# Kernel tuning notes

Hardware: AMD Instinct MI355X
Metric: run time of the kernel (lower is better)

The kernel has to match this reference:

```python
import math
import jax, jax.numpy as jnp
import numpy as np

NEG_INF_FILL = 1e-09  # faithful to the source: masked positions get +1e-09, not -inf

B, H, S, D = 2, 16, 2048, 64


def setup_inputs() -> dict:
    key = jax.random.key(0)
    kq, kk, kv = jax.random.split(key, 3)
    q = jax.random.normal(kq, (B, H, S, D), dtype=jnp.float32)
    k = jax.random.normal(kk, (B, H, S, D), dtype=jnp.float32)
    v = jax.random.normal(kv, (B, H, S, D), dtype=jnp.float32)
    # causal boolean mask, broadcast over heads: [B, 1, S, S]
    causal = jnp.tril(jnp.ones((S, S), dtype=bool))
    attention_mask = jnp.broadcast_to(causal[None, None, :, :], (B, 1, S, S))
    return {"q": q, "k": k, "v": v, "attention_mask": attention_mask}


def reference(q, k, v, attention_mask):
    d_k = q.shape[-1]
    # scores: [B, H, S, S]
    scores = jnp.einsum("bhqd,bhkd->bhqk", q, k) / math.sqrt(d_k)
    scores = jnp.where(attention_mask, scores, NEG_INF_FILL)
    attn = jax.nn.softmax(scores, axis=-1)
    # output: [B, H, S, D]
    return jnp.einsum("bhqk,bhkd->bhqd", attn, v)
```

## Files before the change

### kernel.cpp

```cpp
#include <hip/hip_runtime.h>


#define SEQ 2048
#define DIM 64
#define NKT 32
#define QSCALE 0.18033688011112042f

typedef _Float16 half_t;
typedef _Float16 half8  __attribute__((ext_vector_type(8)));
typedef _Float16 half4v __attribute__((ext_vector_type(4)));
typedef _Float16 half2v __attribute__((ext_vector_type(2)));
typedef float    float4v __attribute__((ext_vector_type(4)));

#define KIMG_HALFS ((size_t)4194304)
#define WS_NEED    ((size_t)17039360)

__device__ __forceinline__ void glds16(const void* g, void* l) {
    __builtin_amdgcn_global_load_lds((const __attribute__((address_space(1))) void*)g,
                                     (__attribute__((address_space(3))) void*)l,
                                     16, 0, 0);
}

__global__ __launch_bounds__(256)
void prep_kernel(const float* __restrict__ K, const float* __restrict__ V,
                 half_t* __restrict__ Kimg, half_t* __restrict__ Vimg) {
    __shared__ __align__(16) half_t vt[64 * 72];
    const int kt = blockIdx.x, bh = blockIdx.y;
    const int tid = threadIdx.x;
    const float* Kt = K + ((size_t)bh * SEQ + kt * 64) * DIM;
    const float* Vt = V + ((size_t)bh * SEQ + kt * 64) * DIM;
    half_t* Kd = Kimg + (((size_t)(bh * NKT + kt)) << 12);
    half_t* Vd = Vimg + (((size_t)(bh * NKT + kt)) << 12);

    {
        const int row = tid >> 2, q = tid & 3;
        const float* src = Kt + row * DIM + 16 * q;
        #pragma unroll
        for (int cc = 0; cc < 2; ++cc) {
            float4v a = *(const float4v*)(src + 8 * cc);
            float4v b = *(const float4v*)(src + 8 * cc + 4);
            half8 hh;
            hh[0]=(half_t)a[0]; hh[1]=(half_t)a[1]; hh[2]=(half_t)a[2]; hh[3]=(half_t)a[3];
            hh[4]=(half_t)b[0]; hh[5]=(half_t)b[1]; hh[6]=(half_t)b[2]; hh[7]=(half_t)b[3];
            const int sc = (2 * q + cc) ^ (row & 7);
            *(half8*)(Kd + row * 64 + sc * 8) = hh;
        }
    }
    {
        const int c = tid & 15, r0 = tid >> 4;
        #pragma unroll
        for (int u = 0; u < 2; ++u) {
            const float* vp = Vt + (size_t)(2 * (r0 + 16 * u)) * DIM + 4 * c;
            float4v x0 = *(const float4v*)(vp);
            float4v x1 = *(const float4v*)(vp + DIM);
            #pragma unroll
            for (int i = 0; i < 4; ++i) {
                const int d = 4 * c + i;
                vt[d * 72 + 2 * (r0 + 16 * u)]     = (half_t)x0[i];
                vt[d * 72 + 2 * (r0 + 16 * u) + 1] = (half_t)x1[i];
            }
        }
    }
    __syncthreads();
    {
        const int d = tid >> 2, g = tid & 3;
        #pragma unroll
        for (int cc = 0; cc < 2; ++cc) {
            const int c0 = 2 * g + cc;
            half8 hh = *(const half8*)(vt + d * 72 + 8 * c0);
            const int sc = c0 ^ (d & 7);
            *(half8*)(Vd + d * 64 + sc * 8) = hh;
        }
    }
}

__global__ __launch_bounds__(256)
void suffix_kernel(const float* __restrict__ V, float* __restrict__ Stab) {
    __shared__ float part[32 * 9];
    const int dg = blockIdx.x, bh = blockIdx.y;
    const int t = threadIdx.x >> 3, dl = threadIdx.x & 7;
    const int d = dg * 8 + dl;
    const float* Vb = V + (size_t)bh * SEQ * DIM;
    float s = 0.f;
    #pragma unroll 8
    for (int j = 0; j < 64; ++j) s += Vb[(size_t)(t * 64 + j) * DIM + d];
    part[t * 9 + dl] = s;
    __syncthreads();
    float r = 0.f;
    for (int tt = 31; tt >= t; --tt) r += part[tt * 9 + dl];
    Stab[((size_t)bh * 32 + t) * 64 + d] = r;
}

__global__ __launch_bounds__(256, 4)
void attn_mfma_kernel(const float* __restrict__ Q,
                      const half_t* __restrict__ Kimg,
                      const half_t* __restrict__ Vimg,
                      const float* __restrict__ Stab,
                      float* __restrict__ O) {
    __shared__ __align__(16) half_t smem_h[20480];

    const int tid = threadIdx.x;
    const int l   = tid & 63;
    const int w   = tid >> 6;
    const int lx  = l & 15;
    const int h   = l >> 4;
    const int bh  = blockIdx.x;
    const int qb  = 31 - (int)blockIdx.y;
    const int qbase = qb * 64;
    const int nkt = qb + 1;
    const int n_tail = SEQ - nkt * 64;

    const float* Qh = Q + (size_t)bh * SEQ * DIM;
    float*       Oh = O + (size_t)bh * SEQ * DIM;

    half8 qf[2];
    const int qrow_w = qbase + 16 * w;
    {
        const float* qp = Qh + (size_t)(qrow_w + lx) * DIM;
        #pragma unroll
        for (int s = 0; s < 2; ++s) {
            float4v a = *(const float4v*)(qp + 32 * s + 8 * h);
            float4v b = *(const float4v*)(qp + 32 * s + 8 * h + 4);
            half8 f;
            f[0] = (half_t)(a[0] * QSCALE); f[1] = (half_t)(a[1] * QSCALE);
            f[2] = (half_t)(a[2] * QSCALE); f[3] = (half_t)(a[3] * QSCALE);
            f[4] = (half_t)(b[0] * QSCALE); f[5] = (half_t)(b[1] * QSCALE);
            f[6] = (half_t)(b[2] * QSCALE); f[7] = (half_t)(b[3] * QSCALE);
            qf[s] = f;
        }
    }

    float4v acc[4];
    #pragma unroll
    for (int mt = 0; mt < 4; ++mt) acc[mt] = (float4v){0.f, 0.f, 0.f, 0.f};
    float lp = 0.f;

    const size_t tile0 = ((size_t)(bh * NKT)) << 13;
    auto stage = [&](int kt, int buf) {
        const size_t toff = tile0 + ((size_t)kt << 13);
        const char* gk = (const char*)Kimg + toff + (tid << 4);
        const char* gv = (const char*)Vimg + toff + (tid << 4);
        char* lk = (char*)smem_h + (buf << 13) + (w << 10);
        char* lv = (char*)smem_h + 16384 + (buf << 13) + (w << 10);
        glds16(gk, lk);  glds16(gk + 4096, lk + 4096);
        glds16(gv, lv);  glds16(gv + 4096, lv + 4096);
    };

    const int sx  = lx & 7;
    const int o0h = (h ^ sx) << 3;
    const int o1h = ((h + 4) ^ sx) << 3;
    half_t* Psw = smem_h + 16384 + (w << 10);

    stage(0, 0);
    asm volatile("s_waitcnt vmcnt(0)" ::: "memory");
    __syncthreads();

    int cur = 0;
    for (int kt = 0; kt < nkt; ++kt) {
        if (kt + 1 < nkt) stage(kt + 1, cur ^ 1);

        const half_t* Kb = smem_h + cur * 4096 + (lx << 6);
        const half_t* Vb = smem_h + 8192 + cur * 4096 + (lx << 6);
        const int key_base = kt << 6;

        #pragma unroll
        for (int mt = 0; mt < 4; ++mt) {
            half8 ak0 = *(const half8*)(Kb + (mt << 10) + o0h);
            half8 ak1 = *(const half8*)(Kb + (mt << 10) + o1h);
            float4v ct = (float4v){0.f, 0.f, 0.f, 0.f};
            ct = __builtin_amdgcn_mfma_f32_16x16x32_f16(ak0, qf[0], ct, 0, 0, 0);
            ct = __builtin_amdgcn_mfma_f32_16x16x32_f16(ak1, qf[1], ct, 0, 0, 0);
            float p[4];
            #pragma unroll
            for (int r = 0; r < 4; ++r)
                p[r] = __builtin_amdgcn_exp2f(ct[r]);
            if ((key_base + 16 * mt + 15) > qrow_w) {
                const int qg = qrow_w + lx;
                const int kb = key_base + 16 * mt + 4 * h;
                #pragma unroll
                for (int r = 0; r < 4; ++r)
                    if (kb + r > qg) p[r] = 1.0f;
            }
            lp += (p[0] + p[1]) + (p[2] + p[3]);
            half4v hp;
            hp[0] = (half_t)p[0]; hp[1] = (half_t)p[1];
            hp[2] = (half_t)p[2]; hp[3] = (half_t)p[3];
            *(half4v*)(Psw + (lx << 6)
                       + ((((mt << 1) + (h >> 1)) ^ sx) << 3) + ((h & 1) << 2)) = hp;
        }

        half8 pf0 = *(const half8*)(Psw + (lx << 6) + o0h);
        half8 pf1 = *(const half8*)(Psw + (lx << 6) + o1h);
        #pragma unroll
        for (int mtd = 0; mtd < 4; ++mtd) {
            half8 av0 = *(const half8*)(Vb + (mtd << 10) + o0h);
            half8 av1 = *(const half8*)(Vb + (mtd << 10) + o1h);
            float4v ct = acc[mtd];
            ct = __builtin_amdgcn_mfma_f32_16x16x32_f16(av0, pf0, ct, 0, 0, 0);
            ct = __builtin_amdgcn_mfma_f32_16x16x32_f16(av1, pf1, ct, 0, 0, 0);
            acc[mtd] = ct;
        }

        asm volatile("s_waitcnt vmcnt(0)" ::: "memory");
        __syncthreads();
        cur ^= 1;
    }

    float s_l = lp;
    s_l += __shfl_xor(s_l, 16, 64);
    s_l += __shfl_xor(s_l, 32, 64);
    const float linv = 1.0f / (s_l + (float)n_tail);

    float vt_l[4][4];
    if (n_tail > 0) {
        const float* Sr = Stab + (((size_t)bh << 5) + nkt) * 64;
        #pragma unroll
        for (int mt = 0; mt < 4; ++mt) {
            float4v x = *(const float4v*)(Sr + 16 * mt + 4 * h);
            vt_l[mt][0] = x[0]; vt_l[mt][1] = x[1];
            vt_l[mt][2] = x[2]; vt_l[mt][3] = x[3];
        }
    } else {
        #pragma unroll
        for (int mt = 0; mt < 4; ++mt)
            vt_l[mt][0] = vt_l[mt][1] = vt_l[mt][2] = vt_l[mt][3] = 0.f;
    }

    float* Osm = (float*)smem_h;
    #pragma unroll
    for (int mt = 0; mt < 4; ++mt)
        #pragma unroll
        for (int r = 0; r < 4; ++r) {
            float o = (acc[mt][r] + vt_l[mt][r]) * linv;
            Osm[w * (16 * 65) + lx * 65 + 16 * mt + 4 * h + r] = o;
        }
    __syncthreads();
    {
        const int c = tid & 15, r0 = tid >> 4;
        #pragma unroll
        for (int u = 0; u < 4; ++u) {
            const int row = r0 + 16 * u;
            const int dc = 4 * c;
            const float* src = Osm + (row >> 4) * (16 * 65) + (row & 15) * 65 + dc;
            float4v ov = {src[0], src[1], src[2], src[3]};
            *(float4v*)(Oh + (size_t)(qbase + row) * DIM + dc) = ov;
        }
    }
}

#define KS_STRIDE 72
#define PS_STRIDE 72

__global__ __launch_bounds__(256, 4)
void attn_mfma_fallback(const float* __restrict__ Q,
                        const float* __restrict__ K,
                        const float* __restrict__ V,
                        float* __restrict__ O) {
    __shared__ half_t smem_h[64 * KS_STRIDE + 64 * KS_STRIDE + 4 * 16 * PS_STRIDE];
    half_t* Ks  = smem_h;
    half_t* VTs = smem_h + 64 * KS_STRIDE;
    half_t* Ps  = smem_h + 2 * 64 * KS_STRIDE;

    const int tid = threadIdx.x;
    const int l   = tid & 63;
    const int w   = tid >> 6;
    const int lx  = l & 15;
    const int h   = l >> 4;
    const int bh  = blockIdx.x;
    const int qb  = 31 - (int)blockIdx.y;
    const int qbase = qb * 64;
    const int nkt = qb + 1;
    const int n_tail = SEQ - nkt * 64;

    const float* Qh = Q + (size_t)bh * SEQ * DIM;
    const float* Kh = K + (size_t)bh * SEQ * DIM;
    const float* Vh = V + (size_t)bh * SEQ * DIM;
    float*       Oh = O + (size_t)bh * SEQ * DIM;

    half8 qf[2];
    const int qrow_w = qbase + 16 * w;
    {
        const float* qp = Qh + (size_t)(qrow_w + lx) * DIM;
        #pragma unroll
        for (int s = 0; s < 2; ++s) {
            float4v a = *(const float4v*)(qp + 32 * s + 8 * h);
            float4v b = *(const float4v*)(qp + 32 * s + 8 * h + 4);
            half8 f;
            f[0] = (half_t)(a[0] * QSCALE); f[1] = (half_t)(a[1] * QSCALE);
            f[2] = (half_t)(a[2] * QSCALE); f[3] = (half_t)(a[3] * QSCALE);
            f[4] = (half_t)(b[0] * QSCALE); f[5] = (half_t)(b[1] * QSCALE);
            f[6] = (half_t)(b[2] * QSCALE); f[7] = (half_t)(b[3] * QSCALE);
            qf[s] = f;
        }
    }

    float4v acc[4];
    #pragma unroll
    for (int mt = 0; mt < 4; ++mt) acc[mt] = (float4v){0.f, 0.f, 0.f, 0.f};
    float lp = 0.f;

    const int c  = tid & 15;
    const int r0 = tid >> 4;

    float4v kreg[4], vreg[4];
    auto load_tile = [&](int kt) {
        const float* Kt = Kh + (size_t)kt * 64 * DIM;
        const float* Vt = Vh + (size_t)kt * 64 * DIM;
        #pragma unroll
        for (int u = 0; u < 4; ++u)
            kreg[u] = *(const float4v*)(Kt + (r0 + 16 * u) * DIM + 4 * c);
        #pragma unroll
        for (int u = 0; u < 2; ++u) {
            const float* vp = Vt + (size_t)(2 * (r0 + 16 * u)) * DIM + 4 * c;
            vreg[2 * u]     = *(const float4v*)(vp);
            vreg[2 * u + 1] = *(const float4v*)(vp + DIM);
        }
    };

    load_tile(0);

    for (int kt = 0; kt < nkt; ++kt) {
        __syncthreads();
        #pragma unroll
        for (int u = 0; u < 4; ++u) {
            int kr = r0 + 16 * u;
            half4v hk;
            hk[0] = (half_t)kreg[u][0]; hk[1] = (half_t)kreg[u][1];
            hk[2] = (half_t)kreg[u][2]; hk[3] = (half_t)kreg[u][3];
            *(half4v*)(Ks + kr * KS_STRIDE + 4 * c) = hk;
        }
        #pragma unroll
        for (int u = 0; u < 2; ++u) {
            int kp = r0 + 16 * u;
            #pragma unroll
            for (int i = 0; i < 4; ++i) {
                int ir = (i + c + (c >> 2)) & 3;
                int dr = 4 * c + ir;
                half2v hv;
                hv[0] = (half_t)vreg[2 * u][ir];
                hv[1] = (half_t)vreg[2 * u + 1][ir];
                *(half2v*)(VTs + dr * KS_STRIDE + 2 * kp) = hv;
            }
        }
        __syncthreads();

        if (kt + 1 < nkt) load_tile(kt + 1);

        const int key_base = kt * 64;
        #pragma unroll
        for (int mt = 0; mt < 4; ++mt) {
            half8 ak0 = *(const half8*)(Ks + (16 * mt + lx) * KS_STRIDE + 8 * h);
            half8 ak1 = *(const half8*)(Ks + (16 * mt + lx) * KS_STRIDE + 32 + 8 * h);
            const bool need_mask = (key_base + 16 * mt + 15) > qrow_w;
            float4v ct = (float4v){0.f, 0.f, 0.f, 0.f};
            ct = __builtin_amdgcn_mfma_f32_16x16x32_f16(ak0, qf[0], ct, 0, 0, 0);
            ct = __builtin_amdgcn_mfma_f32_16x16x32_f16(ak1, qf[1], ct, 0, 0, 0);
            float p[4];
            #pragma unroll
            for (int r = 0; r < 4; ++r)
                p[r] = __builtin_amdgcn_exp2f(ct[r]);
            if (need_mask) {
                const int qg = qrow_w + lx;
                const int kb = key_base + 16 * mt + 4 * h;
                #pragma unroll
                for (int r = 0; r < 4; ++r)
                    if (kb + r > qg) p[r] = 1.0f;
            }
            lp += (p[0] + p[1]) + (p[2] + p[3]);
            half4v hp;
            hp[0] = (half_t)p[0]; hp[1] = (half_t)p[1];
            hp[2] = (half_t)p[2]; hp[3] = (half_t)p[3];
            *(half4v*)(Ps + w * (16 * PS_STRIDE) + lx * PS_STRIDE + 16 * mt + 4 * h) = hp;
        }

        half8 pf[2];
        #pragma unroll
        for (int s = 0; s < 2; ++s)
            pf[s] = *(const half8*)(Ps + w * (16 * PS_STRIDE) + lx * PS_STRIDE
                                    + 32 * s + 8 * h);
        #pragma unroll
        for (int mtd = 0; mtd < 4; ++mtd) {
            half8 av0 = *(const half8*)(VTs + (16 * mtd + lx) * KS_STRIDE + 8 * h);
            half8 av1 = *(const half8*)(VTs + (16 * mtd + lx) * KS_STRIDE + 32 + 8 * h);
            float4v ct = acc[mtd];
            ct = __builtin_amdgcn_mfma_f32_16x16x32_f16(av0, pf[0], ct, 0, 0, 0);
            ct = __builtin_amdgcn_mfma_f32_16x16x32_f16(av1, pf[1], ct, 0, 0, 0);
            acc[mtd] = ct;
        }
    }

    float s_l = lp;
    s_l += __shfl_xor(s_l, 16, 64);
    s_l += __shfl_xor(s_l, 32, 64);
    const float linv = 1.0f / (s_l + (float)n_tail);

    float ts0 = 0.f, ts1 = 0.f, ts2 = 0.f, ts3 = 0.f;
    {
        const int tstart = nkt * 64;
        #pragma unroll 4
        for (int k = tstart + r0; k < SEQ; k += 16) {
            float4v x = *(const float4v*)(Vh + (size_t)k * DIM + 4 * c);
            ts0 += x[0]; ts1 += x[1]; ts2 += x[2]; ts3 += x[3];
        }
    }
    __syncthreads();
    float* preS = (float*)smem_h;
    float* vtf  = ((float*)smem_h) + 4160;
    {
        float4v pv = {ts0, ts1, ts2, ts3};
        *(float4v*)(preS + r0 * 68 + 4 * c) = pv;
    }
    __syncthreads();
    if (tid < 64) {
        float s = 0.f;
        #pragma unroll
        for (int p = 0; p < 16; ++p) s += preS[p * 68 + tid];
        vtf[tid] = s;
    }
    __syncthreads();
    float vt_l[4][4];
    #pragma unroll
    for (int mt = 0; mt < 4; ++mt)
        #pragma unroll
        for (int r = 0; r < 4; ++r) vt_l[mt][r] = vtf[16 * mt + 4 * h + r];

    float* Osm = (float*)smem_h;
    #pragma unroll
    for (int mt = 0; mt < 4; ++mt)
        #pragma unroll
        for (int r = 0; r < 4; ++r) {
            float o = (acc[mt][r] + vt_l[mt][r]) * linv;
            Osm[w * (16 * 65) + lx * 65 + 16 * mt + 4 * h + r] = o;
        }
    __syncthreads();
    #pragma unroll
    for (int u = 0; u < 4; ++u) {
        int row = r0 + 16 * u;
        int dc = 4 * c;
        const float* src = Osm + (row >> 4) * (16 * 65) + (row & 15) * 65 + dc;
        float4v ov = {src[0], src[1], src[2], src[3]};
        *(float4v*)(Oh + (size_t)(qbase + row) * DIM + dc) = ov;
    }
}

extern "C" void kernel_launch(void* const* d_in, const int* in_sizes, int n_in,
                              void* d_out, int out_size, void* d_ws, size_t ws_size,
                              hipStream_t stream) {
    const float* q = (const float*)d_in[0];
    const float* k = (const float*)d_in[1];
    const float* v = (const float*)d_in[2];
    float* out = (float*)d_out;

    if (d_ws != nullptr && ws_size >= WS_NEED) {
        half_t* kimg = (half_t*)d_ws;
        half_t* vimg = kimg + KIMG_HALFS;
        float*  stab = (float*)((char*)d_ws + 16777216);
        prep_kernel<<<dim3(32, 32), 256, 0, stream>>>(k, v, kimg, vimg);
        suffix_kernel<<<dim3(8, 32), 256, 0, stream>>>(v, stab);
        attn_mfma_kernel<<<dim3(32, 32), 256, 0, stream>>>(q, kimg, vimg, stab, out);
    } else {
        attn_mfma_fallback<<<dim3(32, 32), 256, 0, stream>>>(q, k, v, out);
    }
}
```

Baseline: 150.0 us.

## Pair causal query blocks per workgroup and fuse suffix-sum into prep kernel

The attention kernel now runs 512 workgroups, each handling two query blocks (qb = 31-p and qb = p), so every workgroup does the same number of causal key tiles. This replaces a grid of 1024 blocks with very uneven work. The separate suffix-sum kernel is folded into the prep kernel as extra blocks, which removes one launch. In exchange, each workgroup now processes its two query blocks one after the other, and the grid is half as large, which may lower occupancy and latency hiding.

```diff
diff --git a/kernel.cpp b/kernel.cpp
--- a/kernel.cpp
+++ b/kernel.cpp
@@ -23,10 +23,30 @@
 
 __global__ __launch_bounds__(256)
 void prep_kernel(const float* __restrict__ K, const float* __restrict__ V,
-                 half_t* __restrict__ Kimg, half_t* __restrict__ Vimg) {
+                 half_t* __restrict__ Kimg, half_t* __restrict__ Vimg,
+                 float* __restrict__ Stab) {
     __shared__ __align__(16) half_t vt[64 * 72];
-    const int kt = blockIdx.x, bh = blockIdx.y;
+    __shared__ float part[32 * 9];
+    const int bh = blockIdx.y;
     const int tid = threadIdx.x;
+
+    if (blockIdx.x >= NKT) {
+        const int dg = blockIdx.x - NKT;
+        const int t = tid >> 3, dl = tid & 7;
+        const int d = dg * 8 + dl;
+        const float* Vb = V + (size_t)bh * SEQ * DIM;
+        float s = 0.f;
+        #pragma unroll 8
+        for (int j = 0; j < 64; ++j) s += Vb[(size_t)(t * 64 + j) * DIM + d];
+        part[t * 9 + dl] = s;
+        __syncthreads();
+        float r = 0.f;
+        for (int tt = 31; tt >= t; --tt) r += part[tt * 9 + dl];
+        Stab[((size_t)bh * 32 + t) * 64 + d] = r;
+        return;
+    }
+
+    const int kt = blockIdx.x;
     const float* Kt = K + ((size_t)bh * SEQ + kt * 64) * DIM;
     const float* Vt = V + ((size_t)bh * SEQ + kt * 64) * DIM;
     half_t* Kd = Kimg + (((size_t)(bh * NKT + kt)) << 12);
@@ -74,23 +94,6 @@
     }
 }
 
-__global__ __launch_bounds__(256)
-void suffix_kernel(const float* __restrict__ V, float* __restrict__ Stab) {
-    __shared__ float part[32 * 9];
-    const int dg = blockIdx.x, bh = blockIdx.y;
-    const int t = threadIdx.x >> 3, dl = threadIdx.x & 7;
-    const int d = dg * 8 + dl;
-    const float* Vb = V + (size_t)bh * SEQ * DIM;
-    float s = 0.f;
-    #pragma unroll 8
-    for (int j = 0; j < 64; ++j) s += Vb[(size_t)(t * 64 + j) * DIM + d];
-    part[t * 9 + dl] = s;
-    __syncthreads();
-    float r = 0.f;
-    for (int tt = 31; tt >= t; --tt) r += part[tt * 9 + dl];
-    Stab[((size_t)bh * 32 + t) * 64 + d] = r;
-}
-
 __global__ __launch_bounds__(256, 4)
 void attn_mfma_kernel(const float* __restrict__ Q,
                       const half_t* __restrict__ Kimg,
@@ -98,6 +101,173 @@
                       const float* __restrict__ Stab,
                       float* __restrict__ O) {
     __shared__ __align__(16) half_t smem_h[20480];
+
+    const int tid = threadIdx.x;
+    const int l   = tid & 63;
+    const int w   = tid >> 6;
+    const int lx  = l & 15;
+    const int h   = l >> 4;
+    const int bh  = blockIdx.x;
+    const int p   = blockIdx.y;
+
+    const float* Qh = Q + (size_t)bh * SEQ * DIM;
+    float*       Oh = O + (size_t)bh * SEQ * DIM;
+
+    const size_t tile0 = ((size_t)(bh * NKT)) << 13;
+    auto stage = [&](int kt, int buf) {
+        const size_t toff = tile0 + ((size_t)kt << 13);
+        const char* gk = (const char*)Kimg + toff + (tid << 4);
+        const char* gv = (const char*)Vimg + toff + (tid << 4);
+        char* lk = (char*)smem_h + (buf << 13) + (w << 10);
+        char* lv = (char*)smem_h + 16384 + (buf << 13) + (w << 10);
+        glds16(gk, lk);  glds16(gk + 4096, lk + 4096);
+        glds16(gv, lv);  glds16(gv + 4096, lv + 4096);
+    };
+
+    const int sx  = lx & 7;
+    const int o0h = (h ^ sx) << 3;
+    const int o1h = ((h + 4) ^ sx) << 3;
+    half_t* Psw = smem_h + 16384 + (w << 10);
+
+    for (int seg = 0; seg < 2; ++seg) {
+        const int qb    = seg ? p : 31 - p;
+        const int qbase = qb << 6;
+        const int nkt   = qb + 1;
+        const int n_tail = SEQ - (nkt << 6);
+        const int qrow_w = qbase + 16 * w;
+
+        half8 qf[2];
+        {
+            const float* qp = Qh + (size_t)(qrow_w + lx) * DIM;
+            #pragma unroll
+            for (int s = 0; s < 2; ++s) {
+                float4v a = *(const float4v*)(qp + 32 * s + 8 * h);
+                float4v b = *(const float4v*)(qp + 32 * s + 8 * h + 4);
+                half8 f;
+                f[0] = (half_t)(a[0] * QSCALE); f[1] = (half_t)(a[1] * QSCALE);
+                f[2] = (half_t)(a[2] * QSCALE); f[3] = (half_t)(a[3] * QSCALE);
+                f[4] = (half_t)(b[0] * QSCALE); f[5] = (half_t)(b[1] * QSCALE);
+                f[6] = (half_t)(b[2] * QSCALE); f[7] = (half_t)(b[3] * QSCALE);
+                qf[s] = f;
+            }
+        }
+
+        float4v acc[4];
+        #pragma unroll
+        for (int mt = 0; mt < 4; ++mt) acc[mt] = (float4v){0.f, 0.f, 0.f, 0.f};
+        float lp = 0.f;
+
+        __syncthreads();
+        stage(0, 0);
+        asm volatile("s_waitcnt vmcnt(0)" ::: "memory");
+        __syncthreads();
+
+        int cur = 0;
+        for (int kt = 0; kt < nkt; ++kt) {
+            if (kt + 1 < nkt) stage(kt + 1, cur ^ 1);
+
+            const half_t* Kb = smem_h + cur * 4096 + (lx << 6);
+            const half_t* Vb = smem_h + 8192 + cur * 4096 + (lx << 6);
+            const int key_base = kt << 6;
+
+            #pragma unroll
+            for (int mt = 0; mt < 4; ++mt) {
+                half8 ak0 = *(const half8*)(Kb + (mt << 10) + o0h);
+                half8 ak1 = *(const half8*)(Kb + (mt << 10) + o1h);
+                float4v ct = (float4v){0.f, 0.f, 0.f, 0.f};
+                ct = __builtin_amdgcn_mfma_f32_16x16x32_f16(ak0, qf[0], ct, 0, 0, 0);
+                ct = __builtin_amdgcn_mfma_f32_16x16x32_f16(ak1, qf[1], ct, 0, 0, 0);
+                float pv[4];
+                #pragma unroll
+                for (int r = 0; r < 4; ++r)
+                    pv[r] = __builtin_amdgcn_exp2f(ct[r]);
+                if ((key_base + 16 * mt + 15) > qrow_w) {
+                    const int qg = qrow_w + lx;
+                    const int kb = key_base + 16 * mt + 4 * h;
+                    #pragma unroll
+                    for (int r = 0; r < 4; ++r)
+                        if (kb + r > qg) pv[r] = 1.0f;
+                }
+                lp += (pv[0] + pv[1]) + (pv[2] + pv[3]);
+                half4v hp;
+                hp[0] = (half_t)pv[0]; hp[1] = (half_t)pv[1];
+                hp[2] = (half_t)pv[2]; hp[3] = (half_t)pv[3];
+                *(half4v*)(Psw + (lx << 6)
+                           + ((((mt << 1) + (h >> 1)) ^ sx) << 3) + ((h & 1) << 2)) = hp;
+            }
+
+            half8 pf0 = *(const half8*)(Psw + (lx << 6) + o0h);
+            half8 pf1 = *(const half8*)(Psw + (lx << 6) + o1h);
+            #pragma unroll
+            for (int mtd = 0; mtd < 4; ++mtd) {
+                half8 av0 = *(const half8*)(Vb + (mtd << 10) + o0h);
+                half8 av1 = *(const half8*)(Vb + (mtd << 10) + o1h);
+                float4v ct = acc[mtd];
+                ct = __builtin_amdgcn_mfma_f32_16x16x32_f16(av0, pf0, ct, 0, 0, 0);
+                ct = __builtin_amdgcn_mfma_f32_16x16x32_f16(av1, pf1, ct, 0, 0, 0);
+                acc[mtd] = ct;
+            }
+
+            asm volatile("s_waitcnt vmcnt(0)" ::: "memory");
+            __syncthreads();
+            cur ^= 1;
+        }
+
+        float s_l = lp;
+        s_l += __shfl_xor(s_l, 16, 64);
+        s_l += __shfl_xor(s_l, 32, 64);
+        const float linv = 1.0f / (s_l + (float)n_tail);
+
+        float vt_l[4][4];
+        if (n_tail > 0) {
+            const float* Sr = Stab + (((size_t)bh << 5) + nkt) * 64;
+            #pragma unroll
+            for (int mt = 0; mt < 4; ++mt) {
+                float4v x = *(const float4v*)(Sr + 16 * mt + 4 * h);
+                vt_l[mt][0] = x[0]; vt_l[mt][1] = x[1];
+                vt_l[mt][2] = x[2]; vt_l[mt][3] = x[3];
+            }
+        } else {
+            #pragma unroll
+            for (int mt = 0; mt < 4; ++mt)
+                vt_l[mt][0] = vt_l[mt][1] = vt_l[mt][2] = vt_l[mt][3] = 0.f;
+        }
+
+        float* Osm = (float*)smem_h;
+        #pragma unroll
+        for (int mt = 0; mt < 4; ++mt)
+            #pragma unroll
+            for (int r = 0; r < 4; ++r) {
+                float o = (acc[mt][r] + vt_l[mt][r]) * linv;
+                Osm[w * (16 * 65) + lx * 65 + 16 * mt + 4 * h + r] = o;
+            }
+        __syncthreads();
+        {
+            const int c = tid & 15, r0 = tid >> 4;
+            #pragma unroll
+            for (int u = 0; u < 4; ++u) {
+                const int row = r0 + 16 * u;
+                const int dc = 4 * c;
+                const float* src = Osm + (row >> 4) * (16 * 65) + (row & 15) * 65 + dc;
+                float4v ov = {src[0], src[1], src[2], src[3]};
+                *(float4v*)(Oh + (size_t)(qbase + row) * DIM + dc) = ov;
+            }
+        }
+    }
+}
+
+#define KS_STRIDE 72
+#define PS_STRIDE 72
+
+__global__ __launch_bounds__(256, 4)
+void attn_mfma_fallback(const float* __restrict__ Q,
+                        const float* __restrict__ K,
+                        const float* __restrict__ V,
+                        float* __restrict__ O) {
+    __shared__ half_t smem_h[64 * KS_STRIDE + 64 * KS_STRIDE + 4 * 16 * PS_STRIDE];
+    half_t* Ks  = smem_h;
+    half_t* VTs = smem_h + 64 * KS_STRIDE;
+    half_t* Ps  = smem_h + 2 * 64 * KS_STRIDE;
 
     const int tid = threadIdx.x;
     const int l   = tid & 63;
@@ -111,6 +281,8 @@
     const int n_tail = SEQ - nkt * 64;
 
     const float* Qh = Q + (size_t)bh * SEQ * DIM;
+    const float* Kh = K + (size_t)bh * SEQ * DIM;
+    const float* Vh = V + (size_t)bh * SEQ * DIM;
     float*       Oh = O + (size_t)bh * SEQ * DIM;
 
     half8 qf[2];
@@ -135,170 +307,6 @@
     for (int mt = 0; mt < 4; ++mt) acc[mt] = (float4v){0.f, 0.f, 0.f, 0.f};
     float lp = 0.f;
 
-    const size_t tile0 = ((size_t)(bh * NKT)) << 13;
-    auto stage = [&](int kt, int buf) {
-        const size_t toff = tile0 + ((size_t)kt << 13);
-        const char* gk = (const char*)Kimg + toff + (tid << 4);
-        const char* gv = (const char*)Vimg + toff + (tid << 4);
-        char* lk = (char*)smem_h + (buf << 13) + (w << 10);
-        char* lv = (char*)smem_h + 16384 + (buf << 13) + (w << 10);
-        glds16(gk, lk);  glds16(gk + 4096, lk + 4096);
-        glds16(gv, lv);  glds16(gv + 4096, lv + 4096);
-    };
-
-    const int sx  = lx & 7;
-    const int o0h = (h ^ sx) << 3;
-    const int o1h = ((h + 4) ^ sx) << 3;
-    half_t* Psw = smem_h + 16384 + (w << 10);
-
-    stage(0, 0);
-    asm volatile("s_waitcnt vmcnt(0)" ::: "memory");
-    __syncthreads();
-
-    int cur = 0;
-    for (int kt = 0; kt < nkt; ++kt) {
-        if (kt + 1 < nkt) stage(kt + 1, cur ^ 1);
-
-        const half_t* Kb = smem_h + cur * 4096 + (lx << 6);
-        const half_t* Vb = smem_h + 8192 + cur * 4096 + (lx << 6);
-        const int key_base = kt << 6;
-
-        #pragma unroll
-        for (int mt = 0; mt < 4; ++mt) {
-            half8 ak0 = *(const half8*)(Kb + (mt << 10) + o0h);
-            half8 ak1 = *(const half8*)(Kb + (mt << 10) + o1h);
-            float4v ct = (float4v){0.f, 0.f, 0.f, 0.f};
-            ct = __builtin_amdgcn_mfma_f32_16x16x32_f16(ak0, qf[0], ct, 0, 0, 0);
-            ct = __builtin_amdgcn_mfma_f32_16x16x32_f16(ak1, qf[1], ct, 0, 0, 0);
-            float p[4];
-            #pragma unroll
-            for (int r = 0; r < 4; ++r)
-                p[r] = __builtin_amdgcn_exp2f(ct[r]);
-            if ((key_base + 16 * mt + 15) > qrow_w) {
-                const int qg = qrow_w + lx;
-                const int kb = key_base + 16 * mt + 4 * h;
-                #pragma unroll
-                for (int r = 0; r < 4; ++r)
-                    if (kb + r > qg) p[r] = 1.0f;
-            }
-            lp += (p[0] + p[1]) + (p[2] + p[3]);
-            half4v hp;
-            hp[0] = (half_t)p[0]; hp[1] = (half_t)p[1];
-            hp[2] = (half_t)p[2]; hp[3] = (half_t)p[3];
-            *(half4v*)(Psw + (lx << 6)
-                       + ((((mt << 1) + (h >> 1)) ^ sx) << 3) + ((h & 1) << 2)) = hp;
-        }
-
-        half8 pf0 = *(const half8*)(Psw + (lx << 6) + o0h);
-        half8 pf1 = *(const half8*)(Psw + (lx << 6) + o1h);
-        #pragma unroll
-        for (int mtd = 0; mtd < 4; ++mtd) {
-            half8 av0 = *(const half8*)(Vb + (mtd << 10) + o0h);
-            half8 av1 = *(const half8*)(Vb + (mtd << 10) + o1h);
-            float4v ct = acc[mtd];
-            ct = __builtin_amdgcn_mfma_f32_16x16x32_f16(av0, pf0, ct, 0, 0, 0);
-            ct = __builtin_amdgcn_mfma_f32_16x16x32_f16(av1, pf1, ct, 0, 0, 0);
-            acc[mtd] = ct;
-        }
-
-        asm volatile("s_waitcnt vmcnt(0)" ::: "memory");
-        __syncthreads();
-        cur ^= 1;
-    }
-
-    float s_l = lp;
-    s_l += __shfl_xor(s_l, 16, 64);
-    s_l += __shfl_xor(s_l, 32, 64);
-    const float linv = 1.0f / (s_l + (float)n_tail);
-
-    float vt_l[4][4];
-    if (n_tail > 0) {
-        const float* Sr = Stab + (((size_t)bh << 5) + nkt) * 64;
-        #pragma unroll
-        for (int mt = 0; mt < 4; ++mt) {
-            float4v x = *(const float4v*)(Sr + 16 * mt + 4 * h);
-            vt_l[mt][0] = x[0]; vt_l[mt][1] = x[1];
-            vt_l[mt][2] = x[2]; vt_l[mt][3] = x[3];
-        }
-    } else {
-        #pragma unroll
-        for (int mt = 0; mt < 4; ++mt)
-            vt_l[mt][0] = vt_l[mt][1] = vt_l[mt][2] = vt_l[mt][3] = 0.f;
-    }
-
-    float* Osm = (float*)smem_h;
-    #pragma unroll
-    for (int mt = 0; mt < 4; ++mt)
-        #pragma unroll
-        for (int r = 0; r < 4; ++r) {
-            float o = (acc[mt][r] + vt_l[mt][r]) * linv;
-            Osm[w * (16 * 65) + lx * 65 + 16 * mt + 4 * h + r] = o;
-        }
-    __syncthreads();
-    {
-        const int c = tid & 15, r0 = tid >> 4;
-        #pragma unroll
-        for (int u = 0; u < 4; ++u) {
-            const int row = r0 + 16 * u;
-            const int dc = 4 * c;
-            const float* src = Osm + (row >> 4) * (16 * 65) + (row & 15) * 65 + dc;
-            float4v ov = {src[0], src[1], src[2], src[3]};
-            *(float4v*)(Oh + (size_t)(qbase + row) * DIM + dc) = ov;
-        }
-    }
-}
-
-#define KS_STRIDE 72
-#define PS_STRIDE 72
-
-__global__ __launch_bounds__(256, 4)
-void attn_mfma_fallback(const float* __restrict__ Q,
-                        const float* __restrict__ K,
-                        const float* __restrict__ V,
-                        float* __restrict__ O) {
-    __shared__ half_t smem_h[64 * KS_STRIDE + 64 * KS_STRIDE + 4 * 16 * PS_STRIDE];
-    half_t* Ks  = smem_h;
-    half_t* VTs = smem_h + 64 * KS_STRIDE;
-    half_t* Ps  = smem_h + 2 * 64 * KS_STRIDE;
-
-    const int tid = threadIdx.x;
-    const int l   = tid & 63;
-    const int w   = tid >> 6;
-    const int lx  = l & 15;
-    const int h   = l >> 4;
-    const int bh  = blockIdx.x;
-    const int qb  = 31 - (int)blockIdx.y;
-    const int qbase = qb * 64;
-    const int nkt = qb + 1;
-    const int n_tail = SEQ - nkt * 64;
-
-    const float* Qh = Q + (size_t)bh * SEQ * DIM;
-    const float* Kh = K + (size_t)bh * SEQ * DIM;
-    const float* Vh = V + (size_t)bh * SEQ * DIM;
-    float*       Oh = O + (size_t)bh * SEQ * DIM;
-
-    half8 qf[2];
-    const int qrow_w = qbase + 16 * w;
-    {
-        const float* qp = Qh + (size_t)(qrow_w + lx) * DIM;
-        #pragma unroll
-        for (int s = 0; s < 2; ++s) {
-            float4v a = *(const float4v*)(qp + 32 * s + 8 * h);
-            float4v b = *(const float4v*)(qp + 32 * s + 8 * h + 4);
-            half8 f;
-            f[0] = (half_t)(a[0] * QSCALE); f[1] = (half_t)(a[1] * QSCALE);
-            f[2] = (half_t)(a[2] * QSCALE); f[3] = (half_t)(a[3] * QSCALE);
-            f[4] = (half_t)(b[0] * QSCALE); f[5] = (half_t)(b[1] * QSCALE);
-            f[6] = (half_t)(b[2] * QSCALE); f[7] = (half_t)(b[3] * QSCALE);
-            qf[s] = f;
-        }
-    }
-
-    float4v acc[4];
-    #pragma unroll
-    for (int mt = 0; mt < 4; ++mt) acc[mt] = (float4v){0.f, 0.f, 0.f, 0.f};
-    float lp = 0.f;
-
     const int c  = tid & 15;
     const int r0 = tid >> 4;
 
@@ -455,9 +463,8 @@
         half_t* kimg = (half_t*)d_ws;
         half_t* vimg = kimg + KIMG_HALFS;
         float*  stab = (float*)((char*)d_ws + 16777216);
-        prep_kernel<<<dim3(32, 32), 256, 0, stream>>>(k, v, kimg, vimg);
-        suffix_kernel<<<dim3(8, 32), 256, 0, stream>>>(v, stab);
-        attn_mfma_kernel<<<dim3(32, 32), 256, 0, stream>>>(q, kimg, vimg, stab, out);
+        prep_kernel<<<dim3(40, 32), 256, 0, stream>>>(k, v, kimg, vimg, stab);
+        attn_mfma_kernel<<<dim3(32, 16), 256, 0, stream>>>(q, kimg, vimg, stab, out);
     } else {
         attn_mfma_fallback<<<dim3(32, 32), 256, 0, stream>>>(q, k, v, out);
     }
```

Result: no change. 151.5 us (+1.0%).
